# Kernel optimization log

Hardware: AMD Instinct MI355X
Metric: run time of the kernel (lower is better)

Reference implementation:

```python
import jax, jax.numpy as jnp
import numpy as np

N = 200_000           # particles
E = 6_400_000         # neighbor pairs (~32 per particle)
SUPPORT = 0.05
EPS = SUPPORT ** 2 * 0.1
DELTA = 0.1
C0 = 10.0 * float(np.sqrt(2.0 * 9.81 * 0.3))
REST_DENSITY = 1000.0
_KC = 7.0 / float(np.pi)  # 2D Wendland C2 normalization


def kernel_gradient(q, dirs, h):
    # Wendland C2 (2D): W = C/h^2 (1-q)^4 (1+4q), q = r/h in [0,1]
    # dW/dr = C/h^3 * (-20 q (1-q)^3), directed along unit vector dirs
    dkdq = -20.0 * q * (1.0 - q) ** 3 * _KC
    return dirs * (dkdq / h ** 3)[:, None]


def setup_inputs() -> dict:
    key = jax.random.key(0)
    k = jax.random.split(key, 7)
    i = jnp.sort(jax.random.randint(k[0], (E,), 0, N))
    j = jax.random.randint(k[1], (E,), 0, N)
    fluidPosition = jax.random.uniform(k[2], (N, 2), dtype=jnp.float32)
    dx2 = (SUPPORT * 0.5) ** 2
    fluidVolume = dx2 * (1.0 + 0.01 * jax.random.normal(k[3], (N,), dtype=jnp.float32))
    fluidDensity = 0.95 + 0.1 * jax.random.uniform(k[4], (N,), dtype=jnp.float32)
    d = jax.random.normal(k[5], (E, 2), dtype=jnp.float32)
    distances = d / (jnp.linalg.norm(d, axis=1, keepdims=True) + 1e-8)  # unit directions
    radialDistances = jax.random.uniform(k[6], (E,), dtype=jnp.float32, minval=0.05, maxval=1.0)
    return {"fluidPosition": fluidPosition, "fluidVolume": fluidVolume,
            "fluidDensity": fluidDensity, "distances": distances,
            "radialDistances": radialDistances, "i": i, "j": j}


def reference(fluidPosition, fluidVolume, fluidDensity, distances, radialDistances, i, j):
    h = SUPPORT
    n = fluidDensity.shape[0]
    gradW = kernel_gradient(radialDistances, distances, h)          # [E,2]
    r_ba = -distances * (radialDistances * h)[:, None]              # [E,2] displacement
    Vj = fluidVolume[j]

    # --- normalization matrix: sum_j 2 Vj * outer(r_ba, gradW) ---
    term = jnp.einsum('nu,nv->nuv', r_ba, gradW) * (2.0 * Vj)[:, None, None]
    M = jax.ops.segment_sum(term, i, num_segments=n)                # [N,2,2]

    # --- pseudo-inverse + renormalized kernel gradient per edge ---
    Li = jnp.linalg.pinv(M)                                         # [N,2,2]
    grad = jnp.einsum('nuv,nv->nu', Li[i], gradW)                   # [E,2]
    dwij_mag = jnp.sum(jnp.abs(gradW), axis=1)                      # L1 norms
    norm_mag = jnp.sum(jnp.abs(grad), axis=1)
    change = jnp.abs(norm_mag - dwij_mag) / (dwij_mag + 1e-4 * h)
    grad = jnp.where((change < 0.1)[:, None], grad, gradW)

    # --- renormalized density gradient ---
    rho = fluidDensity * REST_DENSITY
    rho_ba = rho[j] - rho[i]
    gradRho = jax.ops.segment_sum((2.0 * rho_ba * Vj)[:, None] * grad, i, num_segments=n)

    # --- deltaSPH density diffusion ---
    rji2 = jnp.sum(r_ba * r_ba, axis=1) + EPS
    densityTerm = 0.5 * jnp.einsum('nu,nu->n', gradRho[i] + gradRho[j], r_ba)
    gradTerm = jnp.einsum('nu,nu->n', gradW, r_ba / rji2[:, None])
    prod = (rho_ba + densityTerm) * gradTerm
    return 2.0 * h * DELTA * C0 * jax.ops.segment_sum(prod * Vj, i, num_segments=n)
```

## Files before the change

### kernel.cpp

```cpp
#include <hip/hip_runtime.h>
#include <hip/hip_fp16.h>
#include <math.h>

#define WAVE   64
#define NPB    32
#define BLOCKT 256
#define SMAX   2

#define KC        2.2281692032865347f
#define H         0.05f
#define INV_H2    400.0f
#define INV_H3    8000.0f
#define EPS_REF   0.00025f
#define K_OUT     0.24261080f
#define REST_RHO  1000.0f

__device__ __forceinline__ float wendland_dkdq(float q) {
    float o = 1.f - q;
    return -20.f * q * o * o * o * KC;
}

union H2F { __half2 h; float f; };
__device__ __forceinline__ float   h2_as_f(__half2 h) { H2F u; u.h = h; return u.f; }
__device__ __forceinline__ __half2 f_as_h2(float f)   { H2F u; u.f = f; return u.h; }

__device__ __forceinline__ int li_search(const int* rp, int e) {
    int lo = 0;
#pragma unroll
    for (int s = NPB / 2; s >= 1; s >>= 1) lo += (rp[lo + s] <= e) ? s : 0;
    return lo;
}

template<int NV>
__device__ __forceinline__ void seg_reduce4(const int k[4], float v[4][NV], float* base) {
    const int lane = threadIdx.x & (WAVE - 1);
    const int k0 = k[0], k3 = k[3];
    const bool split = (k0 != k3);
    const int firstLen  = (k[1]==k0) ? ((k[2]==k0) ? ((k[3]==k0)?4:3) : 2) : 1;
    const int lastStart = (k[2]==k3) ? ((k[1]==k3) ? ((k[0]==k3)?0:1) : 2) : 3;

    float vin[NV], vfirst[NV];
#pragma unroll
    for (int c = 0; c < NV; ++c) {
        float s = v[3][c];
        if (lastStart <= 2) s += v[2][c];
        if (lastStart <= 1) s += v[1][c];
        if (lastStart == 0) s += v[0][c];
        vin[c] = s;
        float f = v[0][c];
        if (firstLen >= 2) f += v[1][c];
        if (firstLen >= 3) f += v[2][c];
        if (firstLen >= 4) f += v[3][c];
        vfirst[c] = f;
    }
#pragma unroll
    for (int idx = 1; idx <= 2; ++idx) {
        if (idx >= firstLen && idx < lastStart && k[idx] >= 0) {
#pragma unroll
            for (int c = 0; c < NV; ++c)
                atomicAdd(base + (size_t)k[idx] * NV + c, v[idx][c]);
        }
    }
    float S[NV];
#pragma unroll
    for (int c = 0; c < NV; ++c) S[c] = vin[c];
    const int klast = k3;
#pragma unroll
    for (int d = 1; d < WAVE; d <<= 1) {
        int okey = __shfl_up(klast, d, WAVE);
        float ov[NV];
#pragma unroll
        for (int c = 0; c < NV; ++c) ov[c] = __shfl_up(S[c], d, WAVE);
        if (lane >= d && okey == klast) {
#pragma unroll
            for (int c = 0; c < NV; ++c) S[c] += ov[c];
        }
    }
    const int prevk = __shfl_up(klast, 1, WAVE);
    float P[NV];
#pragma unroll
    for (int c = 0; c < NV; ++c) P[c] = __shfl_up(S[c], 1, WAVE);
    if (split && k0 >= 0) {
        const bool carry = (lane > 0 && prevk == k0);
#pragma unroll
        for (int c = 0; c < NV; ++c)
            atomicAdd(base + (size_t)k0 * NV + c, vfirst[c] + (carry ? P[c] : 0.f));
    }
    const int nk0 = __shfl_down(k0, 1, WAVE);
    const bool tail = (lane == WAVE - 1) || (nk0 != klast);
    if (tail && klast >= 0) {
#pragma unroll
        for (int c = 0; c < NV; ++c)
            atomicAdd(base + (size_t)klast * NV + c, S[c]);
    }
}

struct EW { int jv[4]; float qv[4], dxv[4], dyv[4]; bool okv[4]; };

__device__ __forceinline__ void load_win(long e0, int beg, int end, int E,
        const int* __restrict__ ej, const float* __restrict__ qarr,
        const float2* __restrict__ dirs, EW& w) {
    if (e0 + 3 < (long)E) {
        int4   j4 = *(const int4*)(ej + e0);
        float4 q4 = *(const float4*)(qarr + e0);
        float4 dA = *(const float4*)((const float*)dirs + 2 * e0);
        float4 dB = *(const float4*)((const float*)dirs + 2 * e0 + 4);
        w.jv[0]=j4.x; w.jv[1]=j4.y; w.jv[2]=j4.z; w.jv[3]=j4.w;
        w.qv[0]=q4.x; w.qv[1]=q4.y; w.qv[2]=q4.z; w.qv[3]=q4.w;
        w.dxv[0]=dA.x; w.dyv[0]=dA.y; w.dxv[1]=dA.z; w.dyv[1]=dA.w;
        w.dxv[2]=dB.x; w.dyv[2]=dB.y; w.dxv[3]=dB.z; w.dyv[3]=dB.w;
    } else {
#pragma unroll
        for (int u = 0; u < 4; ++u) {
            long e = e0 + u;
            if (e < (long)E) {
                w.jv[u] = ej[e]; w.qv[u] = qarr[e];
                float2 d = dirs[e]; w.dxv[u] = d.x; w.dyv[u] = d.y;
            } else { w.jv[u]=0; w.qv[u]=0.f; w.dxv[u]=0.f; w.dyv[u]=0.f; }
        }
    }
#pragma unroll
    for (int u = 0; u < 4; ++u) {
        long e = e0 + u;
        w.okv[u] = (e >= (long)beg) && (e < (long)end);
    }
}

__global__ void k_prep(const int* __restrict__ ei, const float* __restrict__ vol,
                       const float* __restrict__ dens, int* __restrict__ rowptr,
                       float2* __restrict__ vd, int N, int E) {
    int e = blockIdx.x * blockDim.x + threadIdx.x;
    if (e <= E) {
        int prev = (e == 0) ? -1 : ei[e - 1];
        int cur  = (e == E) ? N  : ei[e];
        for (int t = prev + 1; t <= cur; ++t) rowptr[t] = e;
    }
    if (e < N) vd[e] = make_float2(vol[e], dens[e]);
}

__global__ __launch_bounds__(BLOCKT, 4)
void k_AC(const int* __restrict__ ej, const float* __restrict__ qarr,
          const float2* __restrict__ dirs, const float2* __restrict__ vd,
          const int* __restrict__ rowptr, __half2* __restrict__ cst,
          float2* __restrict__ g2, float* __restrict__ outp, int N, int E) {
    __shared__ int    rp[NPB + 1];
    __shared__ float  acc6[NPB * 6];
    __shared__ float  Lild[NPB * 3];
    __shared__ float  gld[NPB * 2];
    __shared__ float2 vdl[NPB];
    const int tid = threadIdx.x;
    const int n0  = blockIdx.x * NPB;
    const int nHi = min(n0 + NPB, N);
    if (tid <= NPB) rp[tid] = rowptr[min(n0 + tid, nHi)];
    if (tid < NPB && n0 + tid < N) vdl[tid] = vd[n0 + tid];
    if (tid < NPB * 6) acc6[tid] = 0.f;
    if (tid < NPB * 2) gld[tid] = 0.f;
    __syncthreads();
    const int  beg = rp[0], end = rp[NPB];
    const long beg4 = (long)beg & ~3L;
    const int  waveBase = tid & ~(WAVE - 1);

    int   li_s[4 * SMAX];
    float w_s[4 * SMAX], dx_s[4 * SMAX], dy_s[4 * SMAX], val_s[4 * SMAX];
#pragma unroll
    for (int x = 0; x < 4 * SMAX; ++x) { li_s[x] = -1; w_s[x]=dx_s[x]=dy_s[x]=val_s[x]=0.f; }

#pragma unroll
    for (int c = 0; c < SMAX; ++c) {
        long ebw = beg4 + ((long)c * BLOCKT + waveBase) * 4;
        if (ebw < (long)end) {
            long e0 = beg4 + ((long)c * BLOCKT + tid) * 4;
            EW wd; load_win(e0, beg, end, E, ej, qarr, dirs, wd);
            const bool all4 = wd.okv[0] && wd.okv[1] && wd.okv[2] && wd.okv[3];
            float4 cpack;
            int k[4]; float v[4][6];
#pragma unroll
            for (int u = 0; u < 4; ++u) {
                k[u] = -1;
#pragma unroll
                for (int c2 = 0; c2 < 6; ++c2) v[u][c2] = 0.f;
                if (wd.okv[u]) {
                    int li = li_search(rp, (int)(e0 + u));
                    float q = wd.qv[u], dx = wd.dxv[u], dy = wd.dyv[u];
                    float2 vdj = vd[wd.jv[u]];
                    float wq = wendland_dkdq(q);
                    float s = -2.f * vdj.x * q * wq * INV_H2;
                    float w = wq * INV_H3;
                    float gwx = dx * w, gwy = dy * w;
                    float rx = -dx * q * H, ry = -dy * q * H;
                    float rji2 = rx * rx + ry * ry + EPS_REF;
                    float gT = (gwx * rx + gwy * ry) / rji2;
                    float gv = gT * vdj.x;
                    float rho_ba = REST_RHO * (vdj.y - vdl[li].y);
                    k[u] = li;
                    v[u][0] = s * dx * dx; v[u][1] = s * dx * dy; v[u][2] = s * dy * dy;
                    v[u][3] = rho_ba * gv; v[u][4] = rx * gv;    v[u][5] = ry * gv;
                    __half2 cp = __floats2half2_rn(0.5f * rx * gv, 0.5f * ry * gv);
                    if (all4) (&cpack.x)[u] = h2_as_f(cp);
                    else      cst[e0 + u] = cp;
                    li_s[c*4+u] = li; w_s[c*4+u] = w;
                    dx_s[c*4+u] = dx; dy_s[c*4+u] = dy;
                    val_s[c*4+u] = 2.f * rho_ba * vdj.x;
                }
            }
            if (all4) ((float4*)cst)[e0 >> 2] = cpack;
            seg_reduce4<6>(k, v, acc6);
        }
    }
    for (int c = SMAX; ; ++c) {
        long ebw = beg4 + ((long)c * BLOCKT + waveBase) * 4;
        if (ebw >= (long)end) break;
        long e0 = beg4 + ((long)c * BLOCKT + tid) * 4;
        EW wd; load_win(e0, beg, end, E, ej, qarr, dirs, wd);
        int k[4]; float v[4][6];
#pragma unroll
        for (int u = 0; u < 4; ++u) {
            k[u] = -1;
#pragma unroll
            for (int c2 = 0; c2 < 6; ++c2) v[u][c2] = 0.f;
            if (wd.okv[u]) {
                int li = li_search(rp, (int)(e0 + u));
                float q = wd.qv[u], dx = wd.dxv[u], dy = wd.dyv[u];
                float2 vdj = vd[wd.jv[u]];
                float wq = wendland_dkdq(q);
                float s = -2.f * vdj.x * q * wq * INV_H2;
                float w = wq * INV_H3;
                float gwx = dx * w, gwy = dy * w;
                float rx = -dx * q * H, ry = -dy * q * H;
                float rji2 = rx * rx + ry * ry + EPS_REF;
                float gT = (gwx * rx + gwy * ry) / rji2;
                float gv = gT * vdj.x;
                float rho_ba = REST_RHO * (vdj.y - vdl[li].y);
                k[u] = li;
                v[u][0] = s * dx * dx; v[u][1] = s * dx * dy; v[u][2] = s * dy * dy;
                v[u][3] = rho_ba * gv; v[u][4] = rx * gv;    v[u][5] = ry * gv;
                cst[e0 + u] = __floats2half2_rn(0.5f * rx * gv, 0.5f * ry * gv);
            }
        }
        seg_reduce4<6>(k, v, acc6);
    }
    __syncthreads();

    if (tid < NPB) {
        float a = acc6[6*tid], b = acc6[6*tid+1], cc = acc6[6*tid+2];
        float half_tr   = 0.5f * (a + cc);
        float half_diff = 0.5f * (a - cc);
        float disc = sqrtf(half_diff * half_diff + b * b);
        float l1 = half_tr + disc, l2 = half_tr - disc;
        float smax = fmaxf(fabsf(l1), fabsf(l2));
        float cutoff = 2.3841858e-6f * smax;
        float i00 = 0.f, i01 = 0.f, i11 = 0.f;
        if (fabsf(l2) > cutoff) {
            float inv = 1.0f / (a * cc - b * b);
            i00 =  cc * inv; i01 = -b * inv; i11 = a * inv;
        } else if (fabsf(l1) > cutoff) {
            float vax = b,       vay = l1 - a;
            float vbx = l1 - cc, vby = b;
            float na = vax*vax + vay*vay, nb = vbx*vbx + vby*vby;
            float vx, vy, n2;
            if (nb >= na) { vx = vbx; vy = vby; n2 = nb; }
            else          { vx = vax; vy = vay; n2 = na; }
            float inv = 1.0f / (l1 * n2);
            i00 = vx*vx*inv; i01 = vx*vy*inv; i11 = vy*vy*inv;
        }
        Lild[3*tid] = i00; Lild[3*tid+1] = i01; Lild[3*tid+2] = i11;
    }
    __syncthreads();

#pragma unroll
    for (int c = 0; c < SMAX; ++c) {
        long ebw = beg4 + ((long)c * BLOCKT + waveBase) * 4;
        if (ebw < (long)end) {
            int k[4]; float v[4][2];
#pragma unroll
            for (int u = 0; u < 4; ++u) {
                int li = li_s[c*4+u];
                k[u] = li; v[u][0] = v[u][1] = 0.f;
                if (li >= 0) {
                    float w = w_s[c*4+u], dx = dx_s[c*4+u], dy = dy_s[c*4+u];
                    float gwx = dx * w, gwy = dy * w;
                    float L0 = Lild[3*li], L1 = Lild[3*li+1], L2v = Lild[3*li+2];
                    float gx = L0 * gwx + L1 * gwy;
                    float gy = L1 * gwx + L2v * gwy;
                    float dm = fabsf(gwx) + fabsf(gwy);
                    float nm = fabsf(gx) + fabsf(gy);
                    float change = fabsf(nm - dm) / (dm + 1e-4f * H);
                    if (!(change < 0.1f)) { gx = gwx; gy = gwy; }
                    v[u][0] = val_s[c*4+u] * gx;
                    v[u][1] = val_s[c*4+u] * gy;
                }
            }
            seg_reduce4<2>(k, v, gld);
        }
    }
    for (int c = SMAX; ; ++c) {
        long ebw = beg4 + ((long)c * BLOCKT + waveBase) * 4;
        if (ebw >= (long)end) break;
        long e0 = beg4 + ((long)c * BLOCKT + tid) * 4;
        EW wd; load_win(e0, beg, end, E, ej, qarr, dirs, wd);
        int k[4]; float v[4][2];
#pragma unroll
        for (int u = 0; u < 4; ++u) {
            k[u] = -1; v[u][0] = v[u][1] = 0.f;
            if (wd.okv[u]) {
                int li = li_search(rp, (int)(e0 + u));
                float q = wd.qv[u], dx = wd.dxv[u], dy = wd.dyv[u];
                float2 vdj = vd[wd.jv[u]];
                float w = wendland_dkdq(q) * INV_H3;
                float gwx = dx * w, gwy = dy * w;
                float L0 = Lild[3*li], L1 = Lild[3*li+1], L2v = Lild[3*li+2];
                float gx = L0 * gwx + L1 * gwy;
                float gy = L1 * gwx + L2v * gwy;
                float dm = fabsf(gwx) + fabsf(gwy);
                float nm = fabsf(gx) + fabsf(gy);
                float change = fabsf(nm - dm) / (dm + 1e-4f * H);
                if (!(change < 0.1f)) { gx = gwx; gy = gwy; }
                float val = 2.f * REST_RHO * (vdj.y - vdl[li].y) * vdj.x;
                k[u] = li; v[u][0] = val * gx; v[u][1] = val * gy;
            }
        }
        seg_reduce4<2>(k, v, gld);
    }
    __syncthreads();
    if (tid < NPB && n0 + tid < N) {
        float gx = gld[2*tid], gy = gld[2*tid+1];
        g2[n0 + tid]   = make_float2(gx, gy);
        outp[n0 + tid] = acc6[6*tid+3] + 0.5f * (gx * acc6[6*tid+4] + gy * acc6[6*tid+5]);
    }
}

__global__ __launch_bounds__(BLOCKT, 4)
void k_D(const int* __restrict__ ej, const __half2* __restrict__ cst,
         const float2* __restrict__ g2, const float* __restrict__ outp,
         const int* __restrict__ rowptr, float* __restrict__ out, int N, int E) {
    __shared__ int   rp[NPB + 1];
    __shared__ float outl[NPB];
    const int tid = threadIdx.x;
    const int n0  = blockIdx.x * NPB;
    const int nHi = min(n0 + NPB, N);
    if (tid <= NPB) rp[tid] = rowptr[min(n0 + tid, nHi)];
    if (tid < NPB) outl[tid] = 0.f;
    __syncthreads();
    const int  beg = rp[0], end = rp[NPB];
    const long beg4 = (long)beg & ~3L;
    const int  waveBase = tid & ~(WAVE - 1);

    for (int c = 0; ; ++c) {
        long ebw = beg4 + ((long)c * BLOCKT + waveBase) * 4;
        if (ebw >= (long)end) break;
        long e0 = beg4 + ((long)c * BLOCKT + tid) * 4;
        int jv[4]; float cv[4]; bool okv[4];
        if (e0 + 3 < (long)E) {
            int4   j4 = *(const int4*)(ej + e0);
            float4 c4 = ((const float4*)cst)[e0 >> 2];
            jv[0]=j4.x; jv[1]=j4.y; jv[2]=j4.z; jv[3]=j4.w;
            cv[0]=c4.x; cv[1]=c4.y; cv[2]=c4.z; cv[3]=c4.w;
        } else {
#pragma unroll
            for (int u = 0; u < 4; ++u) {
                long e = e0 + u;
                if (e < (long)E) { jv[u] = ej[e]; cv[u] = h2_as_f(cst[e]); }
                else             { jv[u] = 0;     cv[u] = 0.f; }
            }
        }
#pragma unroll
        for (int u = 0; u < 4; ++u) {
            long e = e0 + u;
            okv[u] = (e >= (long)beg) && (e < (long)end);
        }
        int k[4]; float v[4][1];
#pragma unroll
        for (int u = 0; u < 4; ++u) {
            k[u] = -1; v[u][0] = 0.f;
            if (okv[u]) {
                int li = li_search(rp, (int)(e0 + u));
                float2 gj = g2[jv[u]];
                __half2 ch = f_as_h2(cv[u]);
                k[u] = li;
                v[u][0] = gj.x * __low2float(ch) + gj.y * __high2float(ch);
            }
        }
        seg_reduce4<1>(k, v, outl);
    }
    __syncthreads();
    if (tid < NPB && n0 + tid < N)
        out[n0 + tid] = K_OUT * (outp[n0 + tid] + outl[tid]);
}

extern "C" void kernel_launch(void* const* d_in, const int* in_sizes, int n_in,
                              void* d_out, int out_size, void* d_ws, size_t ws_size,
                              hipStream_t stream) {
    const float*  vol  = (const float*)d_in[1];
    const float*  dens = (const float*)d_in[2];
    const float2* dirs = (const float2*)d_in[3];
    const float*  qarr = (const float*)d_in[4];
    const int*    ei   = (const int*)d_in[5];
    const int*    ej   = (const int*)d_in[6];
    const int N = in_sizes[1];
    const int E = in_sizes[4];

    size_t off = 0;
    auto alloc = [&](size_t bytes) { void* r = (char*)d_ws + off;
                                     off = (off + bytes + 15) & ~(size_t)15; return r; };
    int*     rowptr = (int*)    alloc((size_t)(N + 1) * 4);
    float2*  vd     = (float2*) alloc((size_t)N * 8);
    float2*  g2     = (float2*) alloc((size_t)N * 8);
    float*   outp   = (float*)  alloc((size_t)N * 4);
    __half2* cst    = (__half2*)alloc((size_t)E * 4);
    float*   out    = (float*)d_out;

    const int tb = 256;
    const int gP = (E + 1 + tb - 1) / tb;
    const int gB = (N + NPB - 1) / NPB;

    k_prep<<<gP, tb, 0, stream>>>(ei, vol, dens, rowptr, vd, N, E);
    k_AC  <<<gB, BLOCKT, 0, stream>>>(ej, qarr, dirs, vd, rowptr, cst, g2, outp, N, E);
    k_D   <<<gB, BLOCKT, 0, stream>>>(ej, cst, g2, outp, rowptr, out, N, E);
}
```

Before: 243.8 us.

## Fuse three kernels into one persistent cooperative kernel with grid syncs and work tickets

Merges the prep, AC and D kernels into one persistent cooperative kernel. A grid-wide sync separates the phases, and an atomic ticket counter hands out 32-particle windows. The wave-level segmented scan reduction is replaced by simple per-thread run-merged shared atomics. Phase D reads ei directly instead of searching the row pointers, and launch bounds rise to 8 blocks per CU. This removes launch gaps and tail imbalance, at the cost of grid-sync overhead, more shared-memory atomic contention and a three-launch fallback path.

```diff
diff --git a/kernel.cpp b/kernel.cpp
--- a/kernel.cpp
+++ b/kernel.cpp
@@ -1,6 +1,9 @@
 #include <hip/hip_runtime.h>
+#include <hip/hip_cooperative_groups.h>
 #include <hip/hip_fp16.h>
 #include <math.h>
+
+namespace cg = cooperative_groups;
 
 #define WAVE   64
 #define NPB    32
@@ -32,66 +35,49 @@
 }
 
 template<int NV>
-__device__ __forceinline__ void seg_reduce4(const int k[4], float v[4][NV], float* base) {
-    const int lane = threadIdx.x & (WAVE - 1);
-    const int k0 = k[0], k3 = k[3];
-    const bool split = (k0 != k3);
-    const int firstLen  = (k[1]==k0) ? ((k[2]==k0) ? ((k[3]==k0)?4:3) : 2) : 1;
-    const int lastStart = (k[2]==k3) ? ((k[1]==k3) ? ((k[0]==k3)?0:1) : 2) : 3;
-
-    float vin[NV], vfirst[NV];
-#pragma unroll
-    for (int c = 0; c < NV; ++c) {
-        float s = v[3][c];
-        if (lastStart <= 2) s += v[2][c];
-        if (lastStart <= 1) s += v[1][c];
-        if (lastStart == 0) s += v[0][c];
-        vin[c] = s;
-        float f = v[0][c];
-        if (firstLen >= 2) f += v[1][c];
-        if (firstLen >= 3) f += v[2][c];
-        if (firstLen >= 4) f += v[3][c];
-        vfirst[c] = f;
-    }
-#pragma unroll
-    for (int idx = 1; idx <= 2; ++idx) {
-        if (idx >= firstLen && idx < lastStart && k[idx] >= 0) {
-#pragma unroll
-            for (int c = 0; c < NV; ++c)
-                atomicAdd(base + (size_t)k[idx] * NV + c, v[idx][c]);
-        }
-    }
-    float S[NV];
-#pragma unroll
-    for (int c = 0; c < NV; ++c) S[c] = vin[c];
-    const int klast = k3;
-#pragma unroll
-    for (int d = 1; d < WAVE; d <<= 1) {
-        int okey = __shfl_up(klast, d, WAVE);
-        float ov[NV];
-#pragma unroll
-        for (int c = 0; c < NV; ++c) ov[c] = __shfl_up(S[c], d, WAVE);
-        if (lane >= d && okey == klast) {
-#pragma unroll
-            for (int c = 0; c < NV; ++c) S[c] += ov[c];
-        }
-    }
-    const int prevk = __shfl_up(klast, 1, WAVE);
-    float P[NV];
-#pragma unroll
-    for (int c = 0; c < NV; ++c) P[c] = __shfl_up(S[c], 1, WAVE);
-    if (split && k0 >= 0) {
-        const bool carry = (lane > 0 && prevk == k0);
-#pragma unroll
-        for (int c = 0; c < NV; ++c)
-            atomicAdd(base + (size_t)k0 * NV + c, vfirst[c] + (carry ? P[c] : 0.f));
-    }
-    const int nk0 = __shfl_down(k0, 1, WAVE);
-    const bool tail = (lane == WAVE - 1) || (nk0 != klast);
-    if (tail && klast >= 0) {
-#pragma unroll
-        for (int c = 0; c < NV; ++c)
-            atomicAdd(base + (size_t)klast * NV + c, S[c]);
+__device__ __forceinline__ void seg_atomic4(const int k[4], float v[4][NV], float* base) {
+    const bool s01 = (k[1] == k[0]);
+    const bool s12 = (k[2] == k[1]);
+    const bool s23 = (k[3] == k[2]);
+    if (k[0] >= 0) {
+        float s[NV];
+#pragma unroll
+        for (int c = 0; c < NV; ++c) {
+            float t = v[0][c];
+            if (s01)               t += v[1][c];
+            if (s01 && s12)        t += v[2][c];
+            if (s01 && s12 && s23) t += v[3][c];
+            s[c] = t;
+        }
+#pragma unroll
+        for (int c = 0; c < NV; ++c) atomicAdd(base + k[0] * NV + c, s[c]);
+    }
+    if (k[1] >= 0 && !s01) {
+        float s[NV];
+#pragma unroll
+        for (int c = 0; c < NV; ++c) {
+            float t = v[1][c];
+            if (s12)        t += v[2][c];
+            if (s12 && s23) t += v[3][c];
+            s[c] = t;
+        }
+#pragma unroll
+        for (int c = 0; c < NV; ++c) atomicAdd(base + k[1] * NV + c, s[c]);
+    }
+    if (k[2] >= 0 && !s12) {
+        float s[NV];
+#pragma unroll
+        for (int c = 0; c < NV; ++c) {
+            float t = v[2][c];
+            if (s23) t += v[3][c];
+            s[c] = t;
+        }
+#pragma unroll
+        for (int c = 0; c < NV; ++c) atomicAdd(base + k[2] * NV + c, s[c]);
+    }
+    if (k[3] >= 0 && !s23) {
+#pragma unroll
+        for (int c = 0; c < NV; ++c) atomicAdd(base + k[3] * NV + c, v[3][c]);
     }
 }
 
@@ -126,265 +112,282 @@
     }
 }
 
-__global__ void k_prep(const int* __restrict__ ei, const float* __restrict__ vol,
-                       const float* __restrict__ dens, int* __restrict__ rowptr,
-                       float2* __restrict__ vd, int N, int E) {
-    int e = blockIdx.x * blockDim.x + threadIdx.x;
-    if (e <= E) {
-        int prev = (e == 0) ? -1 : ei[e - 1];
-        int cur  = (e == E) ? N  : ei[e];
-        for (int t = prev + 1; t <= cur; ++t) rowptr[t] = e;
-    }
-    if (e < N) vd[e] = make_float2(vol[e], dens[e]);
-}
-
-__global__ __launch_bounds__(BLOCKT, 4)
-void k_AC(const int* __restrict__ ej, const float* __restrict__ qarr,
-          const float2* __restrict__ dirs, const float2* __restrict__ vd,
-          const int* __restrict__ rowptr, __half2* __restrict__ cst,
-          float2* __restrict__ g2, float* __restrict__ outp, int N, int E) {
+__global__ __launch_bounds__(BLOCKT, 8)
+void k_fused(const int* __restrict__ ei, const int* __restrict__ ej,
+             const float* __restrict__ qarr, const float2* __restrict__ dirs,
+             const float* __restrict__ vol, const float* __restrict__ dens,
+             int* __restrict__ rowptr, float2* __restrict__ vd,
+             __half2* __restrict__ cst, float2* __restrict__ g2,
+             float* __restrict__ outp, float* __restrict__ out,
+             int* __restrict__ tickets, int N, int E, int nwin, int phase) {
     __shared__ int    rp[NPB + 1];
     __shared__ float  acc6[NPB * 6];
     __shared__ float  Lild[NPB * 3];
     __shared__ float  gld[NPB * 2];
+    __shared__ float  outl[NPB];
     __shared__ float2 vdl[NPB];
+    __shared__ int    wsh;
     const int tid = threadIdx.x;
-    const int n0  = blockIdx.x * NPB;
-    const int nHi = min(n0 + NPB, N);
-    if (tid <= NPB) rp[tid] = rowptr[min(n0 + tid, nHi)];
-    if (tid < NPB && n0 + tid < N) vdl[tid] = vd[n0 + tid];
-    if (tid < NPB * 6) acc6[tid] = 0.f;
-    if (tid < NPB * 2) gld[tid] = 0.f;
-    __syncthreads();
-    const int  beg = rp[0], end = rp[NPB];
-    const long beg4 = (long)beg & ~3L;
-    const int  waveBase = tid & ~(WAVE - 1);
-
-    int   li_s[4 * SMAX];
-    float w_s[4 * SMAX], dx_s[4 * SMAX], dy_s[4 * SMAX], val_s[4 * SMAX];
-#pragma unroll
-    for (int x = 0; x < 4 * SMAX; ++x) { li_s[x] = -1; w_s[x]=dx_s[x]=dy_s[x]=val_s[x]=0.f; }
-
-#pragma unroll
-    for (int c = 0; c < SMAX; ++c) {
-        long ebw = beg4 + ((long)c * BLOCKT + waveBase) * 4;
-        if (ebw < (long)end) {
-            long e0 = beg4 + ((long)c * BLOCKT + tid) * 4;
-            EW wd; load_win(e0, beg, end, E, ej, qarr, dirs, wd);
-            const bool all4 = wd.okv[0] && wd.okv[1] && wd.okv[2] && wd.okv[3];
-            float4 cpack;
-            int k[4]; float v[4][6];
-#pragma unroll
-            for (int u = 0; u < 4; ++u) {
-                k[u] = -1;
-#pragma unroll
-                for (int c2 = 0; c2 < 6; ++c2) v[u][c2] = 0.f;
-                if (wd.okv[u]) {
-                    int li = li_search(rp, (int)(e0 + u));
-                    float q = wd.qv[u], dx = wd.dxv[u], dy = wd.dyv[u];
-                    float2 vdj = vd[wd.jv[u]];
-                    float wq = wendland_dkdq(q);
-                    float s = -2.f * vdj.x * q * wq * INV_H2;
-                    float w = wq * INV_H3;
-                    float gwx = dx * w, gwy = dy * w;
-                    float rx = -dx * q * H, ry = -dy * q * H;
-                    float rji2 = rx * rx + ry * ry + EPS_REF;
-                    float gT = (gwx * rx + gwy * ry) / rji2;
-                    float gv = gT * vdj.x;
-                    float rho_ba = REST_RHO * (vdj.y - vdl[li].y);
-                    k[u] = li;
-                    v[u][0] = s * dx * dx; v[u][1] = s * dx * dy; v[u][2] = s * dy * dy;
-                    v[u][3] = rho_ba * gv; v[u][4] = rx * gv;    v[u][5] = ry * gv;
-                    __half2 cp = __floats2half2_rn(0.5f * rx * gv, 0.5f * ry * gv);
-                    if (all4) (&cpack.x)[u] = h2_as_f(cp);
-                    else      cst[e0 + u] = cp;
-                    li_s[c*4+u] = li; w_s[c*4+u] = w;
-                    dx_s[c*4+u] = dx; dy_s[c*4+u] = dy;
-                    val_s[c*4+u] = 2.f * rho_ba * vdj.x;
-                }
-            }
-            if (all4) ((float4*)cst)[e0 >> 2] = cpack;
-            seg_reduce4<6>(k, v, acc6);
-        }
-    }
-    for (int c = SMAX; ; ++c) {
-        long ebw = beg4 + ((long)c * BLOCKT + waveBase) * 4;
-        if (ebw >= (long)end) break;
-        long e0 = beg4 + ((long)c * BLOCKT + tid) * 4;
-        EW wd; load_win(e0, beg, end, E, ej, qarr, dirs, wd);
-        int k[4]; float v[4][6];
-#pragma unroll
-        for (int u = 0; u < 4; ++u) {
-            k[u] = -1;
-#pragma unroll
-            for (int c2 = 0; c2 < 6; ++c2) v[u][c2] = 0.f;
-            if (wd.okv[u]) {
-                int li = li_search(rp, (int)(e0 + u));
-                float q = wd.qv[u], dx = wd.dxv[u], dy = wd.dyv[u];
-                float2 vdj = vd[wd.jv[u]];
-                float wq = wendland_dkdq(q);
-                float s = -2.f * vdj.x * q * wq * INV_H2;
-                float w = wq * INV_H3;
-                float gwx = dx * w, gwy = dy * w;
-                float rx = -dx * q * H, ry = -dy * q * H;
-                float rji2 = rx * rx + ry * ry + EPS_REF;
-                float gT = (gwx * rx + gwy * ry) / rji2;
-                float gv = gT * vdj.x;
-                float rho_ba = REST_RHO * (vdj.y - vdl[li].y);
-                k[u] = li;
-                v[u][0] = s * dx * dx; v[u][1] = s * dx * dy; v[u][2] = s * dy * dy;
-                v[u][3] = rho_ba * gv; v[u][4] = rx * gv;    v[u][5] = ry * gv;
-                cst[e0 + u] = __floats2half2_rn(0.5f * rx * gv, 0.5f * ry * gv);
-            }
-        }
-        seg_reduce4<6>(k, v, acc6);
-    }
-    __syncthreads();
-
-    if (tid < NPB) {
-        float a = acc6[6*tid], b = acc6[6*tid+1], cc = acc6[6*tid+2];
-        float half_tr   = 0.5f * (a + cc);
-        float half_diff = 0.5f * (a - cc);
-        float disc = sqrtf(half_diff * half_diff + b * b);
-        float l1 = half_tr + disc, l2 = half_tr - disc;
-        float smax = fmaxf(fabsf(l1), fabsf(l2));
-        float cutoff = 2.3841858e-6f * smax;
-        float i00 = 0.f, i01 = 0.f, i11 = 0.f;
-        if (fabsf(l2) > cutoff) {
-            float inv = 1.0f / (a * cc - b * b);
-            i00 =  cc * inv; i01 = -b * inv; i11 = a * inv;
-        } else if (fabsf(l1) > cutoff) {
-            float vax = b,       vay = l1 - a;
-            float vbx = l1 - cc, vby = b;
-            float na = vax*vax + vay*vay, nb = vbx*vbx + vby*vby;
-            float vx, vy, n2;
-            if (nb >= na) { vx = vbx; vy = vby; n2 = nb; }
-            else          { vx = vax; vy = vay; n2 = na; }
-            float inv = 1.0f / (l1 * n2);
-            i00 = vx*vx*inv; i01 = vx*vy*inv; i11 = vy*vy*inv;
-        }
-        Lild[3*tid] = i00; Lild[3*tid+1] = i01; Lild[3*tid+2] = i11;
-    }
-    __syncthreads();
-
-#pragma unroll
-    for (int c = 0; c < SMAX; ++c) {
-        long ebw = beg4 + ((long)c * BLOCKT + waveBase) * 4;
-        if (ebw < (long)end) {
-            int k[4]; float v[4][2];
-#pragma unroll
-            for (int u = 0; u < 4; ++u) {
-                int li = li_s[c*4+u];
-                k[u] = li; v[u][0] = v[u][1] = 0.f;
-                if (li >= 0) {
-                    float w = w_s[c*4+u], dx = dx_s[c*4+u], dy = dy_s[c*4+u];
-                    float gwx = dx * w, gwy = dy * w;
-                    float L0 = Lild[3*li], L1 = Lild[3*li+1], L2v = Lild[3*li+2];
-                    float gx = L0 * gwx + L1 * gwy;
-                    float gy = L1 * gwx + L2v * gwy;
-                    float dm = fabsf(gwx) + fabsf(gwy);
-                    float nm = fabsf(gx) + fabsf(gy);
-                    float change = fabsf(nm - dm) / (dm + 1e-4f * H);
-                    if (!(change < 0.1f)) { gx = gwx; gy = gwy; }
-                    v[u][0] = val_s[c*4+u] * gx;
-                    v[u][1] = val_s[c*4+u] * gy;
-                }
-            }
-            seg_reduce4<2>(k, v, gld);
-        }
-    }
-    for (int c = SMAX; ; ++c) {
-        long ebw = beg4 + ((long)c * BLOCKT + waveBase) * 4;
-        if (ebw >= (long)end) break;
-        long e0 = beg4 + ((long)c * BLOCKT + tid) * 4;
-        EW wd; load_win(e0, beg, end, E, ej, qarr, dirs, wd);
-        int k[4]; float v[4][2];
-#pragma unroll
-        for (int u = 0; u < 4; ++u) {
-            k[u] = -1; v[u][0] = v[u][1] = 0.f;
-            if (wd.okv[u]) {
-                int li = li_search(rp, (int)(e0 + u));
-                float q = wd.qv[u], dx = wd.dxv[u], dy = wd.dyv[u];
-                float2 vdj = vd[wd.jv[u]];
-                float w = wendland_dkdq(q) * INV_H3;
-                float gwx = dx * w, gwy = dy * w;
-                float L0 = Lild[3*li], L1 = Lild[3*li+1], L2v = Lild[3*li+2];
-                float gx = L0 * gwx + L1 * gwy;
-                float gy = L1 * gwx + L2v * gwy;
-                float dm = fabsf(gwx) + fabsf(gwy);
-                float nm = fabsf(gx) + fabsf(gy);
-                float change = fabsf(nm - dm) / (dm + 1e-4f * H);
-                if (!(change < 0.1f)) { gx = gwx; gy = gwy; }
-                float val = 2.f * REST_RHO * (vdj.y - vdl[li].y) * vdj.x;
-                k[u] = li; v[u][0] = val * gx; v[u][1] = val * gy;
-            }
-        }
-        seg_reduce4<2>(k, v, gld);
-    }
-    __syncthreads();
-    if (tid < NPB && n0 + tid < N) {
-        float gx = gld[2*tid], gy = gld[2*tid+1];
-        g2[n0 + tid]   = make_float2(gx, gy);
-        outp[n0 + tid] = acc6[6*tid+3] + 0.5f * (gx * acc6[6*tid+4] + gy * acc6[6*tid+5]);
-    }
-}
-
-__global__ __launch_bounds__(BLOCKT, 4)
-void k_D(const int* __restrict__ ej, const __half2* __restrict__ cst,
-         const float2* __restrict__ g2, const float* __restrict__ outp,
-         const int* __restrict__ rowptr, float* __restrict__ out, int N, int E) {
-    __shared__ int   rp[NPB + 1];
-    __shared__ float outl[NPB];
-    const int tid = threadIdx.x;
-    const int n0  = blockIdx.x * NPB;
-    const int nHi = min(n0 + NPB, N);
-    if (tid <= NPB) rp[tid] = rowptr[min(n0 + tid, nHi)];
-    if (tid < NPB) outl[tid] = 0.f;
-    __syncthreads();
-    const int  beg = rp[0], end = rp[NPB];
-    const long beg4 = (long)beg & ~3L;
-    const int  waveBase = tid & ~(WAVE - 1);
-
-    for (int c = 0; ; ++c) {
-        long ebw = beg4 + ((long)c * BLOCKT + waveBase) * 4;
-        if (ebw >= (long)end) break;
-        long e0 = beg4 + ((long)c * BLOCKT + tid) * 4;
-        int jv[4]; float cv[4]; bool okv[4];
-        if (e0 + 3 < (long)E) {
-            int4   j4 = *(const int4*)(ej + e0);
-            float4 c4 = ((const float4*)cst)[e0 >> 2];
-            jv[0]=j4.x; jv[1]=j4.y; jv[2]=j4.z; jv[3]=j4.w;
-            cv[0]=c4.x; cv[1]=c4.y; cv[2]=c4.z; cv[3]=c4.w;
-        } else {
-#pragma unroll
-            for (int u = 0; u < 4; ++u) {
-                long e = e0 + u;
-                if (e < (long)E) { jv[u] = ej[e]; cv[u] = h2_as_f(cst[e]); }
-                else             { jv[u] = 0;     cv[u] = 0.f; }
-            }
-        }
-#pragma unroll
-        for (int u = 0; u < 4; ++u) {
-            long e = e0 + u;
-            okv[u] = (e >= (long)beg) && (e < (long)end);
-        }
-        int k[4]; float v[4][1];
-#pragma unroll
-        for (int u = 0; u < 4; ++u) {
-            k[u] = -1; v[u][0] = 0.f;
-            if (okv[u]) {
-                int li = li_search(rp, (int)(e0 + u));
-                float2 gj = g2[jv[u]];
-                __half2 ch = f_as_h2(cv[u]);
-                k[u] = li;
-                v[u][0] = gj.x * __low2float(ch) + gj.y * __high2float(ch);
-            }
-        }
-        seg_reduce4<1>(k, v, outl);
-    }
-    __syncthreads();
-    if (tid < NPB && n0 + tid < N)
-        out[n0 + tid] = K_OUT * (outp[n0 + tid] + outl[tid]);
+
+    if (phase <= 0) {
+        for (long e = (long)blockIdx.x * BLOCKT + tid; e <= (long)E;
+             e += (long)gridDim.x * BLOCKT) {
+            int prev = (e == 0)       ? -1 : ei[e - 1];
+            int cur  = (e == (long)E) ? N  : ei[e];
+            for (int t = prev + 1; t <= cur; ++t) rowptr[t] = (int)e;
+        }
+        for (long n = (long)blockIdx.x * BLOCKT + tid; n < (long)N;
+             n += (long)gridDim.x * BLOCKT)
+            vd[n] = make_float2(vol[n], dens[n]);
+        if (blockIdx.x == 0 && tid < 2) tickets[tid] = 0;
+    }
+    if (phase < 0) cg::this_grid().sync();
+
+    if (phase < 0 || phase == 1) {
+        int   li_s[4 * SMAX];
+        float gwx_s[4 * SMAX], gwy_s[4 * SMAX], val_s[4 * SMAX];
+        for (;;) {
+            if (tid == 0) wsh = atomicAdd(&tickets[0], 1);
+            __syncthreads();
+            const int w = wsh;
+            if (w >= nwin) break;
+
+            const int n0  = w * NPB;
+            const int nHi = min(n0 + NPB, N);
+            if (tid <= NPB) rp[tid] = rowptr[min(n0 + tid, nHi)];
+            if (tid < NPB && n0 + tid < N) vdl[tid] = vd[n0 + tid];
+            if (tid < NPB * 6) acc6[tid] = 0.f;
+            if (tid < NPB * 2) gld[tid] = 0.f;
+            __syncthreads();
+            const int  beg = rp[0], end = rp[NPB];
+            const long beg4 = (long)beg & ~3L;
+            const int  waveBase = tid & ~(WAVE - 1);
+
+#pragma unroll
+            for (int x = 0; x < 4 * SMAX; ++x) { li_s[x] = -1; gwx_s[x]=gwy_s[x]=val_s[x]=0.f; }
+
+#pragma unroll
+            for (int c = 0; c < SMAX; ++c) {
+                long ebw = beg4 + ((long)c * BLOCKT + waveBase) * 4;
+                if (ebw < (long)end) {
+                    long e0 = beg4 + ((long)c * BLOCKT + tid) * 4;
+                    EW wd; load_win(e0, beg, end, E, ej, qarr, dirs, wd);
+                    const bool all4 = wd.okv[0] && wd.okv[1] && wd.okv[2] && wd.okv[3];
+                    float4 cpack;
+                    int k[4]; float v[4][6];
+#pragma unroll
+                    for (int u = 0; u < 4; ++u) {
+                        k[u] = -1;
+#pragma unroll
+                        for (int c2 = 0; c2 < 6; ++c2) v[u][c2] = 0.f;
+                        if (wd.okv[u]) {
+                            int li = li_search(rp, (int)(e0 + u));
+                            float q = wd.qv[u], dx = wd.dxv[u], dy = wd.dyv[u];
+                            float2 vdj = vd[wd.jv[u]];
+                            float wq = wendland_dkdq(q);
+                            float s = -2.f * vdj.x * q * wq * INV_H2;
+                            float w2 = wq * INV_H3;
+                            float gwx = dx * w2, gwy = dy * w2;
+                            float rx = -dx * q * H, ry = -dy * q * H;
+                            float rji2 = rx * rx + ry * ry + EPS_REF;
+                            float gT = (gwx * rx + gwy * ry) / rji2;
+                            float gv = gT * vdj.x;
+                            float rho_ba = REST_RHO * (vdj.y - vdl[li].y);
+                            k[u] = li;
+                            v[u][0] = s * dx * dx; v[u][1] = s * dx * dy; v[u][2] = s * dy * dy;
+                            v[u][3] = rho_ba * gv; v[u][4] = rx * gv;    v[u][5] = ry * gv;
+                            __half2 cp = __floats2half2_rn(0.5f * rx * gv, 0.5f * ry * gv);
+                            if (all4) (&cpack.x)[u] = h2_as_f(cp);
+                            else      cst[e0 + u] = cp;
+                            li_s[c*4+u] = li; gwx_s[c*4+u] = gwx; gwy_s[c*4+u] = gwy;
+                            val_s[c*4+u] = 2.f * rho_ba * vdj.x;
+                        }
+                    }
+                    if (all4) ((float4*)cst)[e0 >> 2] = cpack;
+                    seg_atomic4<6>(k, v, acc6);
+                }
+            }
+            for (int c = SMAX; ; ++c) {
+                long ebw = beg4 + ((long)c * BLOCKT + waveBase) * 4;
+                if (ebw >= (long)end) break;
+                long e0 = beg4 + ((long)c * BLOCKT + tid) * 4;
+                EW wd; load_win(e0, beg, end, E, ej, qarr, dirs, wd);
+                int k[4]; float v[4][6];
+#pragma unroll
+                for (int u = 0; u < 4; ++u) {
+                    k[u] = -1;
+#pragma unroll
+                    for (int c2 = 0; c2 < 6; ++c2) v[u][c2] = 0.f;
+                    if (wd.okv[u]) {
+                        int li = li_search(rp, (int)(e0 + u));
+                        float q = wd.qv[u], dx = wd.dxv[u], dy = wd.dyv[u];
+                        float2 vdj = vd[wd.jv[u]];
+                        float wq = wendland_dkdq(q);
+                        float s = -2.f * vdj.x * q * wq * INV_H2;
+                        float w2 = wq * INV_H3;
+                        float gwx = dx * w2, gwy = dy * w2;
+                        float rx = -dx * q * H, ry = -dy * q * H;
+                        float rji2 = rx * rx + ry * ry + EPS_REF;
+                        float gT = (gwx * rx + gwy * ry) / rji2;
+                        float gv = gT * vdj.x;
+                        float rho_ba = REST_RHO * (vdj.y - vdl[li].y);
+                        k[u] = li;
+                        v[u][0] = s * dx * dx; v[u][1] = s * dx * dy; v[u][2] = s * dy * dy;
+                        v[u][3] = rho_ba * gv; v[u][4] = rx * gv;    v[u][5] = ry * gv;
+                        cst[e0 + u] = __floats2half2_rn(0.5f * rx * gv, 0.5f * ry * gv);
+                    }
+                }
+                seg_atomic4<6>(k, v, acc6);
+            }
+            __syncthreads();
+
+            if (tid < NPB) {
+                float a = acc6[6*tid], b = acc6[6*tid+1], cc = acc6[6*tid+2];
+                float half_tr   = 0.5f * (a + cc);
+                float half_diff = 0.5f * (a - cc);
+                float disc = sqrtf(half_diff * half_diff + b * b);
+                float l1 = half_tr + disc, l2 = half_tr - disc;
+                float smax = fmaxf(fabsf(l1), fabsf(l2));
+                float cutoff = 2.3841858e-6f * smax;
+                float i00 = 0.f, i01 = 0.f, i11 = 0.f;
+                if (fabsf(l2) > cutoff) {
+                    float inv = 1.0f / (a * cc - b * b);
+                    i00 =  cc * inv; i01 = -b * inv; i11 = a * inv;
+                } else if (fabsf(l1) > cutoff) {
+                    float vax = b,       vay = l1 - a;
+                    float vbx = l1 - cc, vby = b;
+                    float na = vax*vax + vay*vay, nb = vbx*vbx + vby*vby;
+                    float vx, vy, n2;
+                    if (nb >= na) { vx = vbx; vy = vby; n2 = nb; }
+                    else          { vx = vax; vy = vay; n2 = na; }
+                    float inv = 1.0f / (l1 * n2);
+                    i00 = vx*vx*inv; i01 = vx*vy*inv; i11 = vy*vy*inv;
+                }
+                Lild[3*tid] = i00; Lild[3*tid+1] = i01; Lild[3*tid+2] = i11;
+            }
+            __syncthreads();
+
+#pragma unroll
+            for (int c = 0; c < SMAX; ++c) {
+                long ebw = beg4 + ((long)c * BLOCKT + waveBase) * 4;
+                if (ebw < (long)end) {
+                    int k[4]; float v[4][2];
+#pragma unroll
+                    for (int u = 0; u < 4; ++u) {
+                        int li = li_s[c*4+u];
+                        k[u] = li; v[u][0] = v[u][1] = 0.f;
+                        if (li >= 0) {
+                            float gwx = gwx_s[c*4+u], gwy = gwy_s[c*4+u];
+                            float L0 = Lild[3*li], L1 = Lild[3*li+1], L2v = Lild[3*li+2];
+                            float gx = L0 * gwx + L1 * gwy;
+                            float gy = L1 * gwx + L2v * gwy;
+                            float dm = fabsf(gwx) + fabsf(gwy);
+                            float nm = fabsf(gx) + fabsf(gy);
+                            float change = fabsf(nm - dm) / (dm + 1e-4f * H);
+                            if (!(change < 0.1f)) { gx = gwx; gy = gwy; }
+                            v[u][0] = val_s[c*4+u] * gx;
+                            v[u][1] = val_s[c*4+u] * gy;
+                        }
+                    }
+                    seg_atomic4<2>(k, v, gld);
+                }
+            }
+            for (int c = SMAX; ; ++c) {
+                long ebw = beg4 + ((long)c * BLOCKT + waveBase) * 4;
+                if (ebw >= (long)end) break;
+                long e0 = beg4 + ((long)c * BLOCKT + tid) * 4;
+                EW wd; load_win(e0, beg, end, E, ej, qarr, dirs, wd);
+                int k[4]; float v[4][2];
+#pragma unroll
+                for (int u = 0; u < 4; ++u) {
+                    k[u] = -1; v[u][0] = v[u][1] = 0.f;
+                    if (wd.okv[u]) {
+                        int li = li_search(rp, (int)(e0 + u));
+                        float q = wd.qv[u], dx = wd.dxv[u], dy = wd.dyv[u];
+                        float2 vdj = vd[wd.jv[u]];
+                        float w2 = wendland_dkdq(q) * INV_H3;
+                        float gwx = dx * w2, gwy = dy * w2;
+                        float L0 = Lild[3*li], L1 = Lild[3*li+1], L2v = Lild[3*li+2];
+                        float gx = L0 * gwx + L1 * gwy;
+                        float gy = L1 * gwx + L2v * gwy;
+                        float dm = fabsf(gwx) + fabsf(gwy);
+                        float nm = fabsf(gx) + fabsf(gy);
+                        float change = fabsf(nm - dm) / (dm + 1e-4f * H);
+                        if (!(change < 0.1f)) { gx = gwx; gy = gwy; }
+                        float val = 2.f * REST_RHO * (vdj.y - vdl[li].y) * vdj.x;
+                        k[u] = li; v[u][0] = val * gx; v[u][1] = val * gy;
+                    }
+                }
+                seg_atomic4<2>(k, v, gld);
+            }
+            __syncthreads();
+            if (tid < NPB && n0 + tid < N) {
+                float gx = gld[2*tid], gy = gld[2*tid+1];
+                g2[n0 + tid]   = make_float2(gx, gy);
+                outp[n0 + tid] = acc6[6*tid+3] + 0.5f * (gx * acc6[6*tid+4] + gy * acc6[6*tid+5]);
+            }
+        }
+    }
+    if (phase < 0) cg::this_grid().sync();
+
+    if (phase < 0 || phase == 2) {
+        for (;;) {
+            if (tid == 0) wsh = atomicAdd(&tickets[1], 1);
+            __syncthreads();
+            const int w = wsh;
+            if (w >= nwin) break;
+
+            const int n0  = w * NPB;
+            const int nHi = min(n0 + NPB, N);
+            if (tid < NPB) outl[tid] = 0.f;
+            __syncthreads();
+            const int  beg = rowptr[n0], end = rowptr[nHi];
+            const long beg4 = (long)beg & ~3L;
+            const int  waveBase = tid & ~(WAVE - 1);
+
+            for (int c = 0; ; ++c) {
+                long ebw = beg4 + ((long)c * BLOCKT + waveBase) * 4;
+                if (ebw >= (long)end) break;
+                long e0 = beg4 + ((long)c * BLOCKT + tid) * 4;
+                int iv[4], jv[4]; float cv[4]; bool okv[4];
+                if (e0 + 3 < (long)E) {
+                    int4   i4 = *(const int4*)(ei + e0);
+                    int4   j4 = *(const int4*)(ej + e0);
+                    float4 c4 = ((const float4*)cst)[e0 >> 2];
+                    iv[0]=i4.x; iv[1]=i4.y; iv[2]=i4.z; iv[3]=i4.w;
+                    jv[0]=j4.x; jv[1]=j4.y; jv[2]=j4.z; jv[3]=j4.w;
+                    cv[0]=c4.x; cv[1]=c4.y; cv[2]=c4.z; cv[3]=c4.w;
+                } else {
+#pragma unroll
+                    for (int u = 0; u < 4; ++u) {
+                        long e = e0 + u;
+                        if (e < (long)E) { iv[u] = ei[e]; jv[u] = ej[e]; cv[u] = h2_as_f(cst[e]); }
+                        else             { iv[u] = 0;     jv[u] = 0;     cv[u] = 0.f; }
+                    }
+                }
+#pragma unroll
+                for (int u = 0; u < 4; ++u) {
+                    long e = e0 + u;
+                    okv[u] = (e >= (long)beg) && (e < (long)end);
+                }
+                int k[4]; float v[4][1];
+#pragma unroll
+                for (int u = 0; u < 4; ++u) {
+                    k[u] = -1; v[u][0] = 0.f;
+                    if (okv[u]) {
+                        float2 gj = g2[jv[u]];
+                        __half2 ch = f_as_h2(cv[u]);
+                        k[u] = iv[u] - n0;
+                        v[u][0] = gj.x * __low2float(ch) + gj.y * __high2float(ch);
+                    }
+                }
+                seg_atomic4<1>(k, v, outl);
+            }
+            __syncthreads();
+            if (tid < NPB && n0 + tid < N)
+                out[n0 + tid] = K_OUT * (outp[n0 + tid] + outl[tid]);
+        }
+    }
 }
 
 extern "C" void kernel_launch(void* const* d_in, const int* in_sizes, int n_in,
@@ -398,22 +401,45 @@
     const int*    ej   = (const int*)d_in[6];
     const int N = in_sizes[1];
     const int E = in_sizes[4];
+    const int nwin = (N + NPB - 1) / NPB;
 
     size_t off = 0;
     auto alloc = [&](size_t bytes) { void* r = (char*)d_ws + off;
                                      off = (off + bytes + 15) & ~(size_t)15; return r; };
-    int*     rowptr = (int*)    alloc((size_t)(N + 1) * 4);
-    float2*  vd     = (float2*) alloc((size_t)N * 8);
-    float2*  g2     = (float2*) alloc((size_t)N * 8);
-    float*   outp   = (float*)  alloc((size_t)N * 4);
-    __half2* cst    = (__half2*)alloc((size_t)E * 4);
-    float*   out    = (float*)d_out;
-
-    const int tb = 256;
-    const int gP = (E + 1 + tb - 1) / tb;
-    const int gB = (N + NPB - 1) / NPB;
-
-    k_prep<<<gP, tb, 0, stream>>>(ei, vol, dens, rowptr, vd, N, E);
-    k_AC  <<<gB, BLOCKT, 0, stream>>>(ej, qarr, dirs, vd, rowptr, cst, g2, outp, N, E);
-    k_D   <<<gB, BLOCKT, 0, stream>>>(ej, cst, g2, outp, rowptr, out, N, E);
-}
+    int*     rowptr  = (int*)    alloc((size_t)(N + 1) * 4);
+    float2*  vd      = (float2*) alloc((size_t)N * 8);
+    float2*  g2      = (float2*) alloc((size_t)N * 8);
+    float*   outp    = (float*)  alloc((size_t)N * 4);
+    __half2* cst     = (__half2*)alloc((size_t)E * 4);
+    int*     tickets = (int*)    alloc(2 * sizeof(int));
+    float*   out     = (float*)d_out;
+
+    static int g_grid = 0;
+    if (g_grid == 0) {
+        int dev = 0; (void)hipGetDevice(&dev);
+        hipDeviceProp_t prop;
+        int cus = 256;
+        if (hipGetDeviceProperties(&prop, dev) == hipSuccess) cus = prop.multiProcessorCount;
+        int nb = 0;
+        if (hipOccupancyMaxActiveBlocksPerMultiprocessor(&nb, k_fused, BLOCKT, 0) != hipSuccess || nb < 1)
+            nb = 4;
+        g_grid = nb * cus;
+    }
+
+    int phase = -1;
+    void* args[] = { (void*)&ei, (void*)&ej, (void*)&qarr, (void*)&dirs,
+                     (void*)&vol, (void*)&dens, (void*)&rowptr, (void*)&vd,
+                     (void*)&cst, (void*)&g2, (void*)&outp, (void*)&out,
+                     (void*)&tickets, (void*)&N, (void*)&E, (void*)&nwin, (void*)&phase };
+    hipError_t rc = hipLaunchCooperativeKernel((void*)k_fused, dim3(g_grid), dim3(BLOCKT),
+                                               args, 0, stream);
+    if (rc != hipSuccess) {
+        (void)hipGetLastError();
+        k_fused<<<g_grid, BLOCKT, 0, stream>>>(ei, ej, qarr, dirs, vol, dens, rowptr, vd,
+                                               cst, g2, outp, out, tickets, N, E, nwin, 0);
+        k_fused<<<g_grid, BLOCKT, 0, stream>>>(ei, ej, qarr, dirs, vol, dens, rowptr, vd,
+                                               cst, g2, outp, out, tickets, N, E, nwin, 1);
+        k_fused<<<g_grid, BLOCKT, 0, stream>>>(ei, ej, qarr, dirs, vol, dens, rowptr, vd,
+                                               cst, g2, outp, out, tickets, N, E, nwin, 2);
+    }
+}
```

New measurement: 779.8 us. +219.8%, slower.

## Replace wave-scan segmented reduction with per-thread LDS atomics and hoist gathers

Applied to the files above, without the earlier changes.

Drops the wave-wide shuffle-scan segmented reduction and replaces it with per-thread run merging over four consecutive edges, issuing one shared-memory atomicAdd per run. Neighbor gathers (vd, g2) and row searches are hoisted ahead of the compute loop to expose more memory-level parallelism. Precomputed gradW components are cached in registers instead of w/dx/dy. k_D reads the sorted i array directly in place of the row-pointer binary search. The trade-off is more LDS atomic contention on the same row and an extra global read of i in k_D.

```diff
diff --git a/kernel.cpp b/kernel.cpp
--- a/kernel.cpp
+++ b/kernel.cpp
@@ -32,66 +32,49 @@
 }
 
 template<int NV>
-__device__ __forceinline__ void seg_reduce4(const int k[4], float v[4][NV], float* base) {
-    const int lane = threadIdx.x & (WAVE - 1);
-    const int k0 = k[0], k3 = k[3];
-    const bool split = (k0 != k3);
-    const int firstLen  = (k[1]==k0) ? ((k[2]==k0) ? ((k[3]==k0)?4:3) : 2) : 1;
-    const int lastStart = (k[2]==k3) ? ((k[1]==k3) ? ((k[0]==k3)?0:1) : 2) : 3;
-
-    float vin[NV], vfirst[NV];
-#pragma unroll
-    for (int c = 0; c < NV; ++c) {
-        float s = v[3][c];
-        if (lastStart <= 2) s += v[2][c];
-        if (lastStart <= 1) s += v[1][c];
-        if (lastStart == 0) s += v[0][c];
-        vin[c] = s;
-        float f = v[0][c];
-        if (firstLen >= 2) f += v[1][c];
-        if (firstLen >= 3) f += v[2][c];
-        if (firstLen >= 4) f += v[3][c];
-        vfirst[c] = f;
-    }
-#pragma unroll
-    for (int idx = 1; idx <= 2; ++idx) {
-        if (idx >= firstLen && idx < lastStart && k[idx] >= 0) {
-#pragma unroll
-            for (int c = 0; c < NV; ++c)
-                atomicAdd(base + (size_t)k[idx] * NV + c, v[idx][c]);
-        }
-    }
-    float S[NV];
-#pragma unroll
-    for (int c = 0; c < NV; ++c) S[c] = vin[c];
-    const int klast = k3;
-#pragma unroll
-    for (int d = 1; d < WAVE; d <<= 1) {
-        int okey = __shfl_up(klast, d, WAVE);
-        float ov[NV];
-#pragma unroll
-        for (int c = 0; c < NV; ++c) ov[c] = __shfl_up(S[c], d, WAVE);
-        if (lane >= d && okey == klast) {
-#pragma unroll
-            for (int c = 0; c < NV; ++c) S[c] += ov[c];
-        }
-    }
-    const int prevk = __shfl_up(klast, 1, WAVE);
-    float P[NV];
-#pragma unroll
-    for (int c = 0; c < NV; ++c) P[c] = __shfl_up(S[c], 1, WAVE);
-    if (split && k0 >= 0) {
-        const bool carry = (lane > 0 && prevk == k0);
-#pragma unroll
-        for (int c = 0; c < NV; ++c)
-            atomicAdd(base + (size_t)k0 * NV + c, vfirst[c] + (carry ? P[c] : 0.f));
-    }
-    const int nk0 = __shfl_down(k0, 1, WAVE);
-    const bool tail = (lane == WAVE - 1) || (nk0 != klast);
-    if (tail && klast >= 0) {
-#pragma unroll
-        for (int c = 0; c < NV; ++c)
-            atomicAdd(base + (size_t)klast * NV + c, S[c]);
+__device__ __forceinline__ void seg_atomic4(const int k[4], float v[4][NV], float* base) {
+    const bool s01 = (k[1] == k[0]);
+    const bool s12 = (k[2] == k[1]);
+    const bool s23 = (k[3] == k[2]);
+    if (k[0] >= 0) {
+        float s[NV];
+#pragma unroll
+        for (int c = 0; c < NV; ++c) {
+            float t = v[0][c];
+            if (s01)               t += v[1][c];
+            if (s01 && s12)        t += v[2][c];
+            if (s01 && s12 && s23) t += v[3][c];
+            s[c] = t;
+        }
+#pragma unroll
+        for (int c = 0; c < NV; ++c) atomicAdd(base + k[0] * NV + c, s[c]);
+    }
+    if (k[1] >= 0 && !s01) {
+        float s[NV];
+#pragma unroll
+        for (int c = 0; c < NV; ++c) {
+            float t = v[1][c];
+            if (s12)        t += v[2][c];
+            if (s12 && s23) t += v[3][c];
+            s[c] = t;
+        }
+#pragma unroll
+        for (int c = 0; c < NV; ++c) atomicAdd(base + k[1] * NV + c, s[c]);
+    }
+    if (k[2] >= 0 && !s12) {
+        float s[NV];
+#pragma unroll
+        for (int c = 0; c < NV; ++c) {
+            float t = v[2][c];
+            if (s23) t += v[3][c];
+            s[c] = t;
+        }
+#pragma unroll
+        for (int c = 0; c < NV; ++c) atomicAdd(base + k[2] * NV + c, s[c]);
+    }
+    if (k[3] >= 0 && !s23) {
+#pragma unroll
+        for (int c = 0; c < NV; ++c) atomicAdd(base + k[3] * NV + c, v[3][c]);
     }
 }
 
@@ -161,9 +144,9 @@
     const int  waveBase = tid & ~(WAVE - 1);
 
     int   li_s[4 * SMAX];
-    float w_s[4 * SMAX], dx_s[4 * SMAX], dy_s[4 * SMAX], val_s[4 * SMAX];
-#pragma unroll
-    for (int x = 0; x < 4 * SMAX; ++x) { li_s[x] = -1; w_s[x]=dx_s[x]=dy_s[x]=val_s[x]=0.f; }
+    float gwx_s[4 * SMAX], gwy_s[4 * SMAX], val_s[4 * SMAX];
+#pragma unroll
+    for (int x = 0; x < 4 * SMAX; ++x) { li_s[x] = -1; gwx_s[x]=gwy_s[x]=val_s[x]=0.f; }
 
 #pragma unroll
     for (int c = 0; c < SMAX; ++c) {
@@ -173,6 +156,14 @@
             EW wd; load_win(e0, beg, end, E, ej, qarr, dirs, wd);
             const bool all4 = wd.okv[0] && wd.okv[1] && wd.okv[2] && wd.okv[3];
             float4 cpack;
+            int    li4[4];
+            float2 vdj4[4];
+#pragma unroll
+            for (int u = 0; u < 4; ++u)
+                li4[u] = wd.okv[u] ? li_search(rp, (int)(e0 + u)) : -1;
+#pragma unroll
+            for (int u = 0; u < 4; ++u)
+                vdj4[u] = wd.okv[u] ? vd[wd.jv[u]] : make_float2(0.f, 0.f);
             int k[4]; float v[4][6];
 #pragma unroll
             for (int u = 0; u < 4; ++u) {
@@ -180,9 +171,9 @@
 #pragma unroll
                 for (int c2 = 0; c2 < 6; ++c2) v[u][c2] = 0.f;
                 if (wd.okv[u]) {
-                    int li = li_search(rp, (int)(e0 + u));
+                    int li = li4[u];
                     float q = wd.qv[u], dx = wd.dxv[u], dy = wd.dyv[u];
-                    float2 vdj = vd[wd.jv[u]];
+                    float2 vdj = vdj4[u];
                     float wq = wendland_dkdq(q);
                     float s = -2.f * vdj.x * q * wq * INV_H2;
                     float w = wq * INV_H3;
@@ -198,13 +189,12 @@
                     __half2 cp = __floats2half2_rn(0.5f * rx * gv, 0.5f * ry * gv);
                     if (all4) (&cpack.x)[u] = h2_as_f(cp);
                     else      cst[e0 + u] = cp;
-                    li_s[c*4+u] = li; w_s[c*4+u] = w;
-                    dx_s[c*4+u] = dx; dy_s[c*4+u] = dy;
+                    li_s[c*4+u] = li; gwx_s[c*4+u] = gwx; gwy_s[c*4+u] = gwy;
                     val_s[c*4+u] = 2.f * rho_ba * vdj.x;
                 }
             }
             if (all4) ((float4*)cst)[e0 >> 2] = cpack;
-            seg_reduce4<6>(k, v, acc6);
+            seg_atomic4<6>(k, v, acc6);
         }
     }
     for (int c = SMAX; ; ++c) {
@@ -237,7 +227,7 @@
                 cst[e0 + u] = __floats2half2_rn(0.5f * rx * gv, 0.5f * ry * gv);
             }
         }
-        seg_reduce4<6>(k, v, acc6);
+        seg_atomic4<6>(k, v, acc6);
     }
     __syncthreads();
 
@@ -277,8 +267,7 @@
                 int li = li_s[c*4+u];
                 k[u] = li; v[u][0] = v[u][1] = 0.f;
                 if (li >= 0) {
-                    float w = w_s[c*4+u], dx = dx_s[c*4+u], dy = dy_s[c*4+u];
-                    float gwx = dx * w, gwy = dy * w;
+                    float gwx = gwx_s[c*4+u], gwy = gwy_s[c*4+u];
                     float L0 = Lild[3*li], L1 = Lild[3*li+1], L2v = Lild[3*li+2];
                     float gx = L0 * gwx + L1 * gwy;
                     float gy = L1 * gwx + L2v * gwy;
@@ -290,7 +279,7 @@
                     v[u][1] = val_s[c*4+u] * gy;
                 }
             }
-            seg_reduce4<2>(k, v, gld);
+            seg_atomic4<2>(k, v, gld);
         }
     }
     for (int c = SMAX; ; ++c) {
@@ -319,7 +308,7 @@
                 k[u] = li; v[u][0] = val * gx; v[u][1] = val * gy;
             }
         }
-        seg_reduce4<2>(k, v, gld);
+        seg_atomic4<2>(k, v, gld);
     }
     __syncthreads();
     if (tid < NPB && n0 + tid < N) {
@@ -330,18 +319,17 @@
 }
 
 __global__ __launch_bounds__(BLOCKT, 4)
-void k_D(const int* __restrict__ ej, const __half2* __restrict__ cst,
+void k_D(const int* __restrict__ ei, const int* __restrict__ ej,
+         const __half2* __restrict__ cst,
          const float2* __restrict__ g2, const float* __restrict__ outp,
          const int* __restrict__ rowptr, float* __restrict__ out, int N, int E) {
-    __shared__ int   rp[NPB + 1];
     __shared__ float outl[NPB];
     const int tid = threadIdx.x;
     const int n0  = blockIdx.x * NPB;
     const int nHi = min(n0 + NPB, N);
-    if (tid <= NPB) rp[tid] = rowptr[min(n0 + tid, nHi)];
     if (tid < NPB) outl[tid] = 0.f;
     __syncthreads();
-    const int  beg = rp[0], end = rp[NPB];
+    const int  beg = rowptr[n0], end = rowptr[nHi];
     const long beg4 = (long)beg & ~3L;
     const int  waveBase = tid & ~(WAVE - 1);
 
@@ -349,18 +337,20 @@
         long ebw = beg4 + ((long)c * BLOCKT + waveBase) * 4;
         if (ebw >= (long)end) break;
         long e0 = beg4 + ((long)c * BLOCKT + tid) * 4;
-        int jv[4]; float cv[4]; bool okv[4];
+        int iv[4], jv[4]; float cv[4]; bool okv[4];
         if (e0 + 3 < (long)E) {
+            int4   i4 = *(const int4*)(ei + e0);
             int4   j4 = *(const int4*)(ej + e0);
             float4 c4 = ((const float4*)cst)[e0 >> 2];
+            iv[0]=i4.x; iv[1]=i4.y; iv[2]=i4.z; iv[3]=i4.w;
             jv[0]=j4.x; jv[1]=j4.y; jv[2]=j4.z; jv[3]=j4.w;
             cv[0]=c4.x; cv[1]=c4.y; cv[2]=c4.z; cv[3]=c4.w;
         } else {
 #pragma unroll
             for (int u = 0; u < 4; ++u) {
                 long e = e0 + u;
-                if (e < (long)E) { jv[u] = ej[e]; cv[u] = h2_as_f(cst[e]); }
-                else             { jv[u] = 0;     cv[u] = 0.f; }
+                if (e < (long)E) { iv[u] = ei[e]; jv[u] = ej[e]; cv[u] = h2_as_f(cst[e]); }
+                else             { iv[u] = 0;     jv[u] = 0;     cv[u] = 0.f; }
             }
         }
 #pragma unroll
@@ -368,19 +358,21 @@
             long e = e0 + u;
             okv[u] = (e >= (long)beg) && (e < (long)end);
         }
+        float2 gj4[4];
+#pragma unroll
+        for (int u = 0; u < 4; ++u)
+            gj4[u] = okv[u] ? g2[jv[u]] : make_float2(0.f, 0.f);
         int k[4]; float v[4][1];
 #pragma unroll
         for (int u = 0; u < 4; ++u) {
             k[u] = -1; v[u][0] = 0.f;
             if (okv[u]) {
-                int li = li_search(rp, (int)(e0 + u));
-                float2 gj = g2[jv[u]];
                 __half2 ch = f_as_h2(cv[u]);
-                k[u] = li;
-                v[u][0] = gj.x * __low2float(ch) + gj.y * __high2float(ch);
-            }
-        }
-        seg_reduce4<1>(k, v, outl);
+                k[u] = iv[u] - n0;
+                v[u][0] = gj4[u].x * __low2float(ch) + gj4[u].y * __high2float(ch);
+            }
+        }
+        seg_atomic4<1>(k, v, outl);
     }
     __syncthreads();
     if (tid < NPB && n0 + tid < N)
@@ -415,5 +407,5 @@
 
     k_prep<<<gP, tb, 0, stream>>>(ei, vol, dens, rowptr, vd, N, E);
     k_AC  <<<gB, BLOCKT, 0, stream>>>(ej, qarr, dirs, vd, rowptr, cst, g2, outp, N, E);
-    k_D   <<<gB, BLOCKT, 0, stream>>>(ej, cst, g2, outp, rowptr, out, N, E);
-}
+    k_D   <<<gB, BLOCKT, 0, stream>>>(ei, ej, cst, g2, outp, rowptr, out, N, E);
+}
```

Measured after the change: 302.4 us. +24.0%, slower.
